# Kernel optimization log

Hardware: AMD Instinct MI355X
Metric: run time of the kernel (lower is better)

The kernel has to match this reference:

```python
import jax, jax.numpy as jnp
import numpy as np

N_NODES = 100000


def _gcn_conv(x, W, b, src, dst, norm, n):
    # PyG GCNConv: h = x @ W; out[i] = sum_j norm_ij * h[j]; out += b
    h = x @ W                                   # [N, F_out]
    msg = h[src] * norm[:, None]                # [E_total, F_out] gathered messages
    out = jax.ops.segment_sum(msg, dst, num_segments=n)
    return out + b


def _build_norm(edge_index, n):
    # add self loops, then symmetric normalization deg^-1/2 A_hat deg^-1/2
    loops = jnp.arange(n, dtype=edge_index.dtype)
    src = jnp.concatenate([edge_index[0], loops])
    dst = jnp.concatenate([edge_index[1], loops])
    deg = jnp.zeros((n,), jnp.float32).at[dst].add(1.0)
    dinv = jnp.where(deg > 0, jax.lax.rsqrt(deg), 0.0)
    norm = dinv[src] * dinv[dst]
    return src, dst, norm


def setup_inputs() -> dict:
    key = jax.random.key(0)
    k1, k2, k3 = jax.random.split(key, 3)
    d_in, d_hid, d_out = 128, 128, 64
    x = jax.random.normal(k1, (N_NODES, d_in), jnp.float32)
    edge_index = jax.random.randint(k2, (2, 1600000), 0, N_NODES, jnp.int64)
    kw1, kw2 = jax.random.split(k3)
    W1 = jax.random.normal(kw1, (d_in, d_hid), jnp.float32) * (1.0 / np.sqrt(d_in))
    b1 = jnp.zeros((d_hid,), jnp.float32)
    W2 = jax.random.normal(kw2, (d_hid, d_out), jnp.float32) * (1.0 / np.sqrt(d_hid))
    b2 = jnp.zeros((d_out,), jnp.float32)
    return {"x": x, "edge_index": edge_index, "W1": W1, "b1": b1, "W2": W2, "b2": b2}


def reference(x, edge_index, W1, b1, W2, b2):
    n = x.shape[0]
    src, dst, norm = _build_norm(edge_index, n)
    h = _gcn_conv(x, W1, b1, src, dst, norm, n)
    h = jax.nn.relu(h)
    # F.dropout(training=False) in eval mode is identity
    out = _gcn_conv(h, W2, b2, src, dst, norm, n)
    return out
```

## Files before the change

kernel.cpp:

```cpp
#include <hip/hip_runtime.h>
#include <hip/hip_fp16.h>

typedef _Float16 half8 __attribute__((ext_vector_type(8)));
typedef float f32x4 __attribute__((ext_vector_type(4)));

#define BUCKET_CAP 8192


__device__ __forceinline__ unsigned pack_half2(float x, float y) {
    __half2 h = __float22half2_rn(make_float2(x, y));
    return *reinterpret_cast<unsigned*>(&h);
}
__device__ __forceinline__ float2 up2(unsigned u) {
    __half2 h = *reinterpret_cast<__half2*>(&u);
    return __half22float2(h);
}
__device__ __forceinline__ void acc8(float4& a, uint2 v) {
    float2 p = up2(v.x), q = up2(v.y);
    a.x += p.x; a.y += p.y; a.z += q.x; a.w += q.y;
}
__device__ __forceinline__ void acc4(float2& a, unsigned v) {
    float2 p = up2(v);
    a.x += p.x; a.y += p.y;
}
__device__ __forceinline__ uint2 ld8(const char* __restrict__ b, unsigned off) {
    return *reinterpret_cast<const uint2*>(b + off);
}
__device__ __forceinline__ unsigned ld4(const char* __restrict__ b, unsigned off) {
    return *reinterpret_cast<const unsigned*>(b + off);
}


__global__ __launch_bounds__(256) void k_wconv(const float* __restrict__ W1,
                                               const float* __restrict__ W2,
                                               __half* __restrict__ Wt1,
                                               __half* __restrict__ Wt2,
                                               int* __restrict__ bcnt, int nbz) {
    int i = blockIdx.x * 256 + threadIdx.x;
    if (i < nbz) bcnt[i] = 0;
    if (i < 16384) {
        int col = i >> 7, k = i & 127;
        Wt1[i] = __float2half(W1[(k << 7) + col]);
    } else if (i < 24576) {
        int j = i - 16384;
        int col = j >> 7, k = j & 127;
        Wt2[j] = __float2half(W2[(k << 6) + col]);
    }
}


__global__ __launch_bounds__(256) void k_bscatter2(const int* __restrict__ src,
                                                   const int* __restrict__ dst, int E,
                                                   int* __restrict__ bcnt,
                                                   unsigned* __restrict__ pairs,
                                                   int NB, int epb) {
    __shared__ int h[512];
    __shared__ int base[512];
    for (int i = threadIdx.x; i < NB; i += 256) h[i] = 0;
    __syncthreads();
    int lo = blockIdx.x * epb;
    int hi = min(lo + epb, E);
    for (int e = lo + threadIdx.x; e < hi; e += 256)
        atomicAdd(&h[dst[e] >> 8], 1);
    __syncthreads();
    for (int i = threadIdx.x; i < NB; i += 256) {
        int c = h[i];
        base[i] = c ? atomicAdd(&bcnt[i], c) : 0;
        h[i] = 0;
    }
    __syncthreads();
    for (int e = lo + threadIdx.x; e < hi; e += 256) {
        int s = src[e], d = dst[e];
        int b = d >> 8;
        int r = atomicAdd(&h[b], 1);
        pairs[(size_t)b * BUCKET_CAP + base[b] + r] =
            (unsigned)s | ((unsigned)(d & 255) << 24);
    }
}

__global__ __launch_bounds__(256) void k_bfinal2(const unsigned* __restrict__ pairs,
                                                 const int* __restrict__ bcnt,
                                                 float* __restrict__ dinv,
                                                 int* __restrict__ offs,
                                                 int* __restrict__ csc,
                                                 int n, int E, int NB) {
    __shared__ int cnt[256];
    __shared__ int scn[256];
    int b = blockIdx.x, t = threadIdx.x;

    int part = 0;
    for (int i = t; i < b; i += 256) part += bcnt[i];
    scn[t] = part;
    __syncthreads();
    for (int d = 128; d > 0; d >>= 1) {
        if (t < d) scn[t] += scn[t + d];
        __syncthreads();
    }
    int cbase = scn[0];
    int cnt_b = bcnt[b];
    __syncthreads();

    cnt[t] = 0;
    __syncthreads();
    size_t plo = (size_t)b * BUCKET_CAP;
    for (int e = t; e < cnt_b; e += 256)
        atomicAdd(&cnt[pairs[plo + e] >> 24], 1);
    __syncthreads();
    int c = cnt[t];
    int node = b * 256 + t;
    if (node < n) dinv[node] = rsqrtf((float)(c + 1));
    scn[t] = c;
    __syncthreads();
    for (int d = 1; d < 256; d <<= 1) {
        int xv = (t >= d) ? scn[t - d] : 0;
        __syncthreads();
        scn[t] += xv;
        __syncthreads();
    }
    int myoff = cbase + scn[t] - c;
    if (node < n) offs[node] = myoff;
    if (b == NB - 1 && t == 255) offs[n] = cbase + scn[255];
    cnt[t] = myoff;
    __syncthreads();
    for (int e = t; e < cnt_b; e += 256) {
        unsigned p = pairs[plo + e];
        int pos = atomicAdd(&cnt[p >> 24], 1);
        csc[pos] = (int)(p & 0x00FFFFFFu);
    }
}


__global__ __launch_bounds__(256) void gemm1_mfma(const float* __restrict__ X,
                                                  const __half* __restrict__ Wt,
                                                  const float* __restrict__ dinv,
                                                  __half* __restrict__ H, int nrows) {
    __shared__ half8 wt[2048];
    const int t = threadIdx.x;

    const half8* Wg = reinterpret_cast<const half8*>(Wt);
    for (int i = t; i < 2048; i += 256) {
        int col = i >> 4, kc = i & 15;
        wt[(col << 4) | (kc ^ (col & 7))] = Wg[i];
    }

    const int wid = t >> 6, lane = t & 63;
    const int li = lane & 15, kq = lane >> 4;
    const int rbase = blockIdx.x * 64 + wid * 16;
    int row = rbase + li;
    int rowc = min(row, nrows - 1);

    const f32x4* X4 = reinterpret_cast<const f32x4*>(X) + (size_t)rowc * 32;
    half8 a[4];
#pragma unroll
    for (int kk = 0; kk < 4; ++kk) {
        f32x4 lo = __builtin_nontemporal_load(&X4[kk * 8 + kq * 2]);
        f32x4 hi = __builtin_nontemporal_load(&X4[kk * 8 + kq * 2 + 1]);
        half8 v;
        v[0] = (_Float16)lo[0]; v[1] = (_Float16)lo[1];
        v[2] = (_Float16)lo[2]; v[3] = (_Float16)lo[3];
        v[4] = (_Float16)hi[0]; v[5] = (_Float16)hi[1];
        v[6] = (_Float16)hi[2]; v[7] = (_Float16)hi[3];
        a[kk] = v;
    }
    __syncthreads();

    f32x4 acc[8];
#pragma unroll
    for (int ct = 0; ct < 8; ++ct) acc[ct] = (f32x4){0.f, 0.f, 0.f, 0.f};

#pragma unroll
    for (int ct = 0; ct < 8; ++ct) {
        int col = ct * 16 + li;
        int cbase = col << 4, sw = col & 7;
#pragma unroll
        for (int kk = 0; kk < 4; ++kk) {
            half8 b = wt[cbase | ((kk * 4 + kq) ^ sw)];
            acc[ct] = __builtin_amdgcn_mfma_f32_16x16x32_f16(a[kk], b, acc[ct], 0, 0, 0);
        }
    }

    const int r0 = rbase + kq * 4;
#pragma unroll
    for (int r = 0; r < 4; ++r) {
        int rr = r0 + r;
        if (rr < nrows) {
            float s = dinv[rr];
            __half* orow = H + (size_t)rr * 128;
#pragma unroll
            for (int ct = 0; ct < 8; ++ct)
                orow[ct * 16 + li] = __float2half(acc[ct][r] * s);
        }
    }
}

__global__ __launch_bounds__(256) void gemm2_mfma(const __half* __restrict__ Xh,
                                                  const __half* __restrict__ Wt,
                                                  const float* __restrict__ dinv,
                                                  __half* __restrict__ H, int nrows) {
    __shared__ half8 wt[1024];
    const int t = threadIdx.x;

    const half8* Wg = reinterpret_cast<const half8*>(Wt);
    for (int i = t; i < 1024; i += 256) {
        int col = i >> 4, kc = i & 15;
        wt[(col << 4) | (kc ^ (col & 7))] = Wg[i];
    }

    const int wid = t >> 6, lane = t & 63;
    const int li = lane & 15, kq = lane >> 4;
    const int rbase = blockIdx.x * 64 + wid * 16;
    int row = rbase + li;
    int rowc = min(row, nrows - 1);

    const half8* A8 = reinterpret_cast<const half8*>(Xh) + (size_t)rowc * 16;
    half8 a[4];
#pragma unroll
    for (int kk = 0; kk < 4; ++kk) a[kk] = A8[kk * 4 + kq];
    __syncthreads();

    f32x4 acc[4];
#pragma unroll
    for (int ct = 0; ct < 4; ++ct) acc[ct] = (f32x4){0.f, 0.f, 0.f, 0.f};

#pragma unroll
    for (int ct = 0; ct < 4; ++ct) {
        int col = ct * 16 + li;
        int cbase = col << 4, sw = col & 7;
#pragma unroll
        for (int kk = 0; kk < 4; ++kk) {
            half8 b = wt[cbase | ((kk * 4 + kq) ^ sw)];
            acc[ct] = __builtin_amdgcn_mfma_f32_16x16x32_f16(a[kk], b, acc[ct], 0, 0, 0);
        }
    }

    const int r0 = rbase + kq * 4;
#pragma unroll
    for (int r = 0; r < 4; ++r) {
        int rr = r0 + r;
        if (rr < nrows) {
            float s = dinv[rr];
            __half* orow = H + (size_t)rr * 64;
#pragma unroll
            for (int ct = 0; ct < 4; ++ct)
                orow[ct * 16 + li] = __float2half(acc[ct][r] * s);
        }
    }
}


__global__ __launch_bounds__(256) void k_agg1(const __half* __restrict__ h,
                                              const int* __restrict__ offs,
                                              const int* __restrict__ csc,
                                              const float* __restrict__ dinv,
                                              const float* __restrict__ bias,
                                              __half* __restrict__ out, int n) {
    int node = (blockIdx.x * 256 + threadIdx.x) >> 6;
    if (node >= n) return;
    int lane = threadIdx.x & 63;
    int g = lane >> 5, li = lane & 31;
    const char* hb = reinterpret_cast<const char*>(h);
    const unsigned loff = (unsigned)li << 3;
    int start = __builtin_amdgcn_readfirstlane(offs[node]);
    int end   = __builtin_amdgcn_readfirstlane(offs[node + 1]);
    float4 acc = make_float4(0.f, 0.f, 0.f, 0.f);

    int e = start;
    int emain = start + ((end - start) & ~15);
    for (; e < emain; e += 16) {
        int idx[16];
#pragma unroll
        for (int j = 0; j < 16; ++j) idx[j] = csc[e + j];
        uint2 v[8];
#pragma unroll
        for (int j = 0; j < 8; ++j)
            v[j] = ld8(hb, (((unsigned)(g ? idx[2 * j + 1] : idx[2 * j])) << 8) | loff);
#pragma unroll
        for (int j = 0; j < 8; ++j) acc8(acc, v[j]);
    }
    for (; e < end; e += 2) {
        int sa = csc[e];
        int sb = (e + 1 < end) ? csc[e + 1] : sa;
        unsigned o = (((unsigned)(g ? sb : sa)) << 8) | loff;
        uint2 v = ld8(hb, o);
        if (g && (e + 1 >= end)) { v.x = 0u; v.y = 0u; }
        acc8(acc, v);
    }
    acc.x += __shfl_xor(acc.x, 32);
    acc.y += __shfl_xor(acc.y, 32);
    acc.z += __shfl_xor(acc.z, 32);
    acc.w += __shfl_xor(acc.w, 32);
    uint2 vs = ld8(hb, (((unsigned)node) << 8) | loff);
    acc8(acc, vs);
    float di = dinv[node];
    float4 bb = reinterpret_cast<const float4*>(bias)[li];
    float ox = fmaxf(fmaf(acc.x, di, bb.x), 0.f);
    float oy = fmaxf(fmaf(acc.y, di, bb.y), 0.f);
    float oz = fmaxf(fmaf(acc.z, di, bb.z), 0.f);
    float ow = fmaxf(fmaf(acc.w, di, bb.w), 0.f);
    if (g == 0)
        reinterpret_cast<uint2*>(out)[(size_t)node * 32 + li] =
            make_uint2(pack_half2(ox, oy), pack_half2(oz, ow));
}

__global__ __launch_bounds__(256) void k_agg2(const __half* __restrict__ h,
                                              const int* __restrict__ offs,
                                              const int* __restrict__ csc,
                                              const float* __restrict__ dinv,
                                              const float* __restrict__ bias,
                                              float* __restrict__ out, int n) {
    int node = (blockIdx.x * 256 + threadIdx.x) >> 6;
    if (node >= n) return;
    int lane = threadIdx.x & 63;
    int g = lane >> 5, li = lane & 31;
    const char* hb = reinterpret_cast<const char*>(h);
    const unsigned loff = (unsigned)li << 2;
    int start = __builtin_amdgcn_readfirstlane(offs[node]);
    int end   = __builtin_amdgcn_readfirstlane(offs[node + 1]);
    float2 acc = make_float2(0.f, 0.f);

    int e = start;
    int emain = start + ((end - start) & ~15);
    for (; e < emain; e += 16) {
        int idx[16];
#pragma unroll
        for (int j = 0; j < 16; ++j) idx[j] = csc[e + j];
        unsigned v[8];
#pragma unroll
        for (int j = 0; j < 8; ++j)
            v[j] = ld4(hb, (((unsigned)(g ? idx[2 * j + 1] : idx[2 * j])) << 7) | loff);
#pragma unroll
        for (int j = 0; j < 8; ++j) acc4(acc, v[j]);
    }
    for (; e < end; e += 2) {
        int sa = csc[e];
        int sb = (e + 1 < end) ? csc[e + 1] : sa;
        unsigned o = (((unsigned)(g ? sb : sa)) << 7) | loff;
        unsigned v = ld4(hb, o);
        if (g && (e + 1 >= end)) v = 0u;
        acc4(acc, v);
    }
    acc.x += __shfl_xor(acc.x, 32);
    acc.y += __shfl_xor(acc.y, 32);
    acc4(acc, ld4(hb, (((unsigned)node) << 7) | loff));
    float di = dinv[node];
    float2 bb = reinterpret_cast<const float2*>(bias)[li];
    if (g == 0)
        reinterpret_cast<float2*>(out)[(size_t)node * 32 + li] =
            make_float2(fmaf(acc.x, di, bb.x), fmaf(acc.y, di, bb.y));
}


extern "C" void kernel_launch(void* const* d_in, const int* in_sizes, int n_in,
                              void* d_out, int out_size, void* d_ws, size_t ws_size,
                              hipStream_t stream) {
    const float* x  = (const float*)d_in[0];
    const int*   ei = (const int*)d_in[1];
    const float* W1 = (const float*)d_in[2];
    const float* b1 = (const float*)d_in[3];
    const float* W2 = (const float*)d_in[4];
    const float* b2 = (const float*)d_in[5];
    float* out = (float*)d_out;

    const int n = in_sizes[0] / 128;
    const int E = in_sizes[1] / 2;
    const int* src = ei;
    const int* dst = ei + E;
    const int NB = (n + 255) / 256;

    char* p = (char*)d_ws;
    auto carve = [&](size_t bytes) -> void* {
        void* r = (void*)p;
        p += (bytes + 255) & ~(size_t)255;
        return r;
    };
    float* dinv    = (float*)carve((size_t)n * 4);
    int*   offs    = (int*)carve((size_t)(n + 1) * 4);
    int*   bcnt    = (int*)carve((size_t)(NB + 1) * 4);
    __half* Wt1h   = (__half*)carve(16384 * 2);
    __half* Wt2h   = (__half*)carve(8192 * 2);
    int*   csc     = (int*)carve((size_t)E * 4);
    __half* h1     = (__half*)carve((size_t)n * 128 * 2);
    __half* out1   = (__half*)carve((size_t)n * 128 * 2);
    unsigned* pairs = (unsigned*)h1;
    __half* h2     = h1;

    const int gmm  = (n + 63) / 64;
    const int gagg = (n + 3) / 4;
    const int GB   = 256;
    const int epb  = (E + GB - 1) / GB;

    k_wconv<<<96, 256, 0, stream>>>(W1, W2, Wt1h, Wt2h, bcnt, NB + 1);

    k_bscatter2<<<GB, 256, 0, stream>>>(src, dst, E, bcnt, pairs, NB, epb);
    k_bfinal2<<<NB, 256, 0, stream>>>(pairs, bcnt, dinv, offs, csc, n, E, NB);

    gemm1_mfma<<<gmm, 256, 0, stream>>>(x, Wt1h, dinv, h1, n);
    k_agg1<<<gagg, 256, 0, stream>>>(h1, offs, csc, dinv, b1, out1, n);

    gemm2_mfma<<<gmm, 256, 0, stream>>>(out1, Wt2h, dinv, h2, n);
    k_agg2<<<gagg, 256, 0, stream>>>(h2, offs, csc, dinv, b2, out, n);
}
```

Measured before the change: 220.5 us.

## Use 1024-node dst buckets for CSC build and shorten gather unroll

The CSC build now groups destination nodes into 1024-node buckets instead of 256. Each packed pair holds a 17-bit source index plus a 10-bit local destination, and each finalize thread handles four nodes with vectorized offs/dinv stores. The scatter grid grows to 512 blocks, and both aggregation kernels drop their gather unroll from 16 edges to 8 to lower register pressure. The risks are fewer finalize blocks (less parallelism), fewer loads in flight per wave in aggregation, and a packing that only holds when node counts stay below 2^17.

New measurement: 203.5 us. 1.08x faster.

```diff
diff --git a/kernel.cpp b/kernel.cpp
--- a/kernel.cpp
+++ b/kernel.cpp
@@ -4,7 +4,9 @@
 typedef _Float16 half8 __attribute__((ext_vector_type(8)));
 typedef float f32x4 __attribute__((ext_vector_type(4)));
 
-#define BUCKET_CAP 8192
+#define BUCKET_CAP 32768
+#define BNODES 1024
+#define NBSHIFT 10
 
 
 __device__ __forceinline__ unsigned pack_half2(float x, float y) {
@@ -54,14 +56,14 @@
                                                    int* __restrict__ bcnt,
                                                    unsigned* __restrict__ pairs,
                                                    int NB, int epb) {
-    __shared__ int h[512];
-    __shared__ int base[512];
+    __shared__ int h[128];
+    __shared__ int base[128];
     for (int i = threadIdx.x; i < NB; i += 256) h[i] = 0;
     __syncthreads();
     int lo = blockIdx.x * epb;
     int hi = min(lo + epb, E);
     for (int e = lo + threadIdx.x; e < hi; e += 256)
-        atomicAdd(&h[dst[e] >> 8], 1);
+        atomicAdd(&h[dst[e] >> NBSHIFT], 1);
     __syncthreads();
     for (int i = threadIdx.x; i < NB; i += 256) {
         int c = h[i];
@@ -71,10 +73,10 @@
     __syncthreads();
     for (int e = lo + threadIdx.x; e < hi; e += 256) {
         int s = src[e], d = dst[e];
-        int b = d >> 8;
+        int b = d >> NBSHIFT;
         int r = atomicAdd(&h[b], 1);
         pairs[(size_t)b * BUCKET_CAP + base[b] + r] =
-            (unsigned)s | ((unsigned)(d & 255) << 24);
+            (unsigned)s | ((unsigned)(d & (BNODES - 1)) << 17);
     }
 }
 
@@ -84,8 +86,9 @@
                                                  int* __restrict__ offs,
                                                  int* __restrict__ csc,
                                                  int n, int E, int NB) {
-    __shared__ int cnt[256];
+    __shared__ int cnt[BNODES];
     __shared__ int scn[256];
+    __shared__ int cur[BNODES];
     int b = blockIdx.x, t = threadIdx.x;
 
     int part = 0;
@@ -100,16 +103,17 @@
     int cnt_b = bcnt[b];
     __syncthreads();
 
-    cnt[t] = 0;
+    for (int i = t; i < BNODES; i += 256) cnt[i] = 0;
     __syncthreads();
     size_t plo = (size_t)b * BUCKET_CAP;
     for (int e = t; e < cnt_b; e += 256)
-        atomicAdd(&cnt[pairs[plo + e] >> 24], 1);
-    __syncthreads();
-    int c = cnt[t];
-    int node = b * 256 + t;
-    if (node < n) dinv[node] = rsqrtf((float)(c + 1));
-    scn[t] = c;
+        atomicAdd(&cnt[pairs[plo + e] >> 17], 1);
+    __syncthreads();
+
+    int c0 = cnt[4 * t], c1 = cnt[4 * t + 1], c2 = cnt[4 * t + 2], c3 = cnt[4 * t + 3];
+    int tot = c0 + c1 + c2 + c3;
+    __syncthreads();
+    scn[t] = tot;
     __syncthreads();
     for (int d = 1; d < 256; d <<= 1) {
         int xv = (t >= d) ? scn[t - d] : 0;
@@ -117,15 +121,26 @@
         scn[t] += xv;
         __syncthreads();
     }
-    int myoff = cbase + scn[t] - c;
-    if (node < n) offs[node] = myoff;
-    if (b == NB - 1 && t == 255) offs[n] = cbase + scn[255];
-    cnt[t] = myoff;
+    int basee = cbase + scn[t] - tot;
+    int o0 = basee, o1 = basee + c0, o2 = o1 + c1, o3 = o2 + c2;
+    int node0 = b * BNODES + 4 * t;
+    if (node0 + 3 < n) {
+        *reinterpret_cast<int4*>(offs + node0) = make_int4(o0, o1, o2, o3);
+        *reinterpret_cast<float4*>(dinv + node0) =
+            make_float4(rsqrtf((float)(c0 + 1)), rsqrtf((float)(c1 + 1)),
+                        rsqrtf((float)(c2 + 1)), rsqrtf((float)(c3 + 1)));
+    } else {
+        if (node0 < n)     { offs[node0]     = o0; dinv[node0]     = rsqrtf((float)(c0 + 1)); }
+        if (node0 + 1 < n) { offs[node0 + 1] = o1; dinv[node0 + 1] = rsqrtf((float)(c1 + 1)); }
+        if (node0 + 2 < n) { offs[node0 + 2] = o2; dinv[node0 + 2] = rsqrtf((float)(c2 + 1)); }
+    }
+    if (b == NB - 1 && t == 255) offs[n] = E;
+    cur[4 * t] = o0; cur[4 * t + 1] = o1; cur[4 * t + 2] = o2; cur[4 * t + 3] = o3;
     __syncthreads();
     for (int e = t; e < cnt_b; e += 256) {
         unsigned p = pairs[plo + e];
-        int pos = atomicAdd(&cnt[p >> 24], 1);
-        csc[pos] = (int)(p & 0x00FFFFFFu);
+        int pos = atomicAdd(&cur[p >> 17], 1);
+        csc[pos] = (int)(p & 0x1FFFFu);
     }
 }
 
@@ -265,17 +280,19 @@
     float4 acc = make_float4(0.f, 0.f, 0.f, 0.f);
 
     int e = start;
-    int emain = start + ((end - start) & ~15);
-    for (; e < emain; e += 16) {
-        int idx[16];
-#pragma unroll
-        for (int j = 0; j < 16; ++j) idx[j] = csc[e + j];
-        uint2 v[8];
-#pragma unroll
-        for (int j = 0; j < 8; ++j)
-            v[j] = ld8(hb, (((unsigned)(g ? idx[2 * j + 1] : idx[2 * j])) << 8) | loff);
-#pragma unroll
-        for (int j = 0; j < 8; ++j) acc8(acc, v[j]);
+    int emain = start + ((end - start) & ~7);
+    for (; e < emain; e += 8) {
+        int a0 = csc[e],     a1 = csc[e + 1], a2 = csc[e + 2], a3 = csc[e + 3];
+        int a4 = csc[e + 4], a5 = csc[e + 5], a6 = csc[e + 6], a7 = csc[e + 7];
+        unsigned o0 = (((unsigned)(g ? a1 : a0)) << 8) | loff;
+        unsigned o1 = (((unsigned)(g ? a3 : a2)) << 8) | loff;
+        unsigned o2 = (((unsigned)(g ? a5 : a4)) << 8) | loff;
+        unsigned o3 = (((unsigned)(g ? a7 : a6)) << 8) | loff;
+        uint2 v0 = ld8(hb, o0);
+        uint2 v1 = ld8(hb, o1);
+        uint2 v2 = ld8(hb, o2);
+        uint2 v3 = ld8(hb, o3);
+        acc8(acc, v0); acc8(acc, v1); acc8(acc, v2); acc8(acc, v3);
     }
     for (; e < end; e += 2) {
         int sa = csc[e];
@@ -319,17 +336,19 @@
     float2 acc = make_float2(0.f, 0.f);
 
     int e = start;
-    int emain = start + ((end - start) & ~15);
-    for (; e < emain; e += 16) {
-        int idx[16];
-#pragma unroll
-        for (int j = 0; j < 16; ++j) idx[j] = csc[e + j];
-        unsigned v[8];
-#pragma unroll
-        for (int j = 0; j < 8; ++j)
-            v[j] = ld4(hb, (((unsigned)(g ? idx[2 * j + 1] : idx[2 * j])) << 7) | loff);
-#pragma unroll
-        for (int j = 0; j < 8; ++j) acc4(acc, v[j]);
+    int emain = start + ((end - start) & ~7);
+    for (; e < emain; e += 8) {
+        int a0 = csc[e],     a1 = csc[e + 1], a2 = csc[e + 2], a3 = csc[e + 3];
+        int a4 = csc[e + 4], a5 = csc[e + 5], a6 = csc[e + 6], a7 = csc[e + 7];
+        unsigned o0 = (((unsigned)(g ? a1 : a0)) << 7) | loff;
+        unsigned o1 = (((unsigned)(g ? a3 : a2)) << 7) | loff;
+        unsigned o2 = (((unsigned)(g ? a5 : a4)) << 7) | loff;
+        unsigned o3 = (((unsigned)(g ? a7 : a6)) << 7) | loff;
+        unsigned v0 = ld4(hb, o0);
+        unsigned v1 = ld4(hb, o1);
+        unsigned v2 = ld4(hb, o2);
+        unsigned v3 = ld4(hb, o3);
+        acc4(acc, v0); acc4(acc, v1); acc4(acc, v2); acc4(acc, v3);
     }
     for (; e < end; e += 2) {
         int sa = csc[e];
@@ -365,7 +384,7 @@
     const int E = in_sizes[1] / 2;
     const int* src = ei;
     const int* dst = ei + E;
-    const int NB = (n + 255) / 256;
+    const int NB = (n + BNODES - 1) / BNODES;
 
     char* p = (char*)d_ws;
     auto carve = [&](size_t bytes) -> void* {
@@ -386,7 +405,7 @@
 
     const int gmm  = (n + 63) / 64;
     const int gagg = (n + 3) / 4;
-    const int GB   = 256;
+    const int GB   = 512;
     const int epb  = (E + GB - 1) / GB;
 
     k_wconv<<<96, 256, 0, stream>>>(W1, W2, Wt1h, Wt2h, bcnt, NB + 1);
```

## Store hidden features in 16-column slices and aggregate per slice for cache locality

Applied to the files above, without the earlier changes.

The GEMM outputs and the layer-1 aggregation output now use a sliced layout: 16-feature (32-byte) slices, each holding all nodes contiguously. The aggregation kernels launch one block per slice and node group, with 16 edges per wavefront gathered in parallel. Each slice's working set is smaller, so random neighbour gathers should hit L2/MALL more often. The cost is 8x more blocks, repeated index loads per slice, and 32-byte gathers that may use memory transactions less efficiently. The last offset is also set directly to E.

Result: slower. 422.7 us (+91.7%).

```diff
diff --git a/kernel.cpp b/kernel.cpp
--- a/kernel.cpp
+++ b/kernel.cpp
@@ -19,15 +19,8 @@
     float2 p = up2(v.x), q = up2(v.y);
     a.x += p.x; a.y += p.y; a.z += q.x; a.w += q.y;
 }
-__device__ __forceinline__ void acc4(float2& a, unsigned v) {
-    float2 p = up2(v);
-    a.x += p.x; a.y += p.y;
-}
 __device__ __forceinline__ uint2 ld8(const char* __restrict__ b, unsigned off) {
     return *reinterpret_cast<const uint2*>(b + off);
-}
-__device__ __forceinline__ unsigned ld4(const char* __restrict__ b, unsigned off) {
-    return *reinterpret_cast<const unsigned*>(b + off);
 }
 
 
@@ -119,7 +112,7 @@
     }
     int myoff = cbase + scn[t] - c;
     if (node < n) offs[node] = myoff;
-    if (b == NB - 1 && t == 255) offs[n] = cbase + scn[255];
+    if (b == NB - 1 && t == 255) offs[n] = E;
     cnt[t] = myoff;
     __syncthreads();
     for (int e = t; e < cnt_b; e += 256) {
@@ -133,7 +126,7 @@
 __global__ __launch_bounds__(256) void gemm1_mfma(const float* __restrict__ X,
                                                   const __half* __restrict__ Wt,
                                                   const float* __restrict__ dinv,
-                                                  __half* __restrict__ H, int nrows) {
+                                                  __half* __restrict__ H, int nrows, int N) {
     __shared__ half8 wt[2048];
     const int t = threadIdx.x;
 
@@ -179,16 +172,18 @@
         }
     }
 
+    char* Hb = reinterpret_cast<char*>(H);
     const int r0 = rbase + kq * 4;
 #pragma unroll
     for (int r = 0; r < 4; ++r) {
         int rr = r0 + r;
         if (rr < nrows) {
             float s = dinv[rr];
-            __half* orow = H + (size_t)rr * 128;
-#pragma unroll
-            for (int ct = 0; ct < 8; ++ct)
-                orow[ct * 16 + li] = __float2half(acc[ct][r] * s);
+#pragma unroll
+            for (int ct = 0; ct < 8; ++ct) {
+                size_t off = ((size_t)ct * N + rr) * 32 + li * 2;
+                *reinterpret_cast<__half*>(Hb + off) = __float2half(acc[ct][r] * s);
+            }
         }
     }
 }
@@ -196,7 +191,8 @@
 __global__ __launch_bounds__(256) void gemm2_mfma(const __half* __restrict__ Xh,
                                                   const __half* __restrict__ Wt,
                                                   const float* __restrict__ dinv,
-                                                  __half* __restrict__ H, int nrows) {
+                                                  __half* __restrict__ H,
+                                                  int nrows, int N) {
     __shared__ half8 wt[1024];
     const int t = threadIdx.x;
 
@@ -212,10 +208,14 @@
     int row = rbase + li;
     int rowc = min(row, nrows - 1);
 
-    const half8* A8 = reinterpret_cast<const half8*>(Xh) + (size_t)rowc * 16;
+    const char* Xb = reinterpret_cast<const char*>(Xh);
     half8 a[4];
 #pragma unroll
-    for (int kk = 0; kk < 4; ++kk) a[kk] = A8[kk * 4 + kq];
+    for (int kk = 0; kk < 4; ++kk) {
+        int f0 = (kk * 4 + kq) * 8;
+        size_t off = ((size_t)(f0 >> 4) * N + rowc) * 32 + (f0 & 15) * 2;
+        a[kk] = *reinterpret_cast<const half8*>(Xb + off);
+    }
     __syncthreads();
 
     f32x4 acc[4];
@@ -233,120 +233,127 @@
         }
     }
 
+    char* Hb = reinterpret_cast<char*>(H);
     const int r0 = rbase + kq * 4;
 #pragma unroll
     for (int r = 0; r < 4; ++r) {
         int rr = r0 + r;
         if (rr < nrows) {
             float s = dinv[rr];
-            __half* orow = H + (size_t)rr * 64;
-#pragma unroll
-            for (int ct = 0; ct < 4; ++ct)
-                orow[ct * 16 + li] = __float2half(acc[ct][r] * s);
+#pragma unroll
+            for (int ct = 0; ct < 4; ++ct) {
+                size_t off = ((size_t)ct * N + rr) * 32 + li * 2;
+                *reinterpret_cast<__half*>(Hb + off) = __float2half(acc[ct][r] * s);
+            }
         }
     }
 }
 
 
-__global__ __launch_bounds__(256) void k_agg1(const __half* __restrict__ h,
-                                              const int* __restrict__ offs,
-                                              const int* __restrict__ csc,
-                                              const float* __restrict__ dinv,
-                                              const float* __restrict__ bias,
-                                              __half* __restrict__ out, int n) {
-    int node = (blockIdx.x * 256 + threadIdx.x) >> 6;
+__global__ __launch_bounds__(256) void k_agg1s(const __half* __restrict__ h,
+                                               const int* __restrict__ offs,
+                                               const int* __restrict__ csc,
+                                               const float* __restrict__ dinv,
+                                               const float* __restrict__ bias,
+                                               __half* __restrict__ out,
+                                               int n, int N) {
+    const int bid = blockIdx.x;
+    const int slice = bid & 7;
+    const int wid = (threadIdx.x >> 6);
+    const int node = (bid >> 3) * 4 + wid;
     if (node >= n) return;
-    int lane = threadIdx.x & 63;
-    int g = lane >> 5, li = lane & 31;
-    const char* hb = reinterpret_cast<const char*>(h);
-    const unsigned loff = (unsigned)li << 3;
+    const int lane = threadIdx.x & 63;
+    const int eg = lane >> 2;
+    const int lb = lane & 3;
+    const unsigned loff = (unsigned)lb << 3;
+
+    const char* hsl = reinterpret_cast<const char*>(h) + (size_t)slice * ((size_t)N * 32);
     int start = __builtin_amdgcn_readfirstlane(offs[node]);
     int end   = __builtin_amdgcn_readfirstlane(offs[node + 1]);
+
     float4 acc = make_float4(0.f, 0.f, 0.f, 0.f);
-
-    int e = start;
-    int emain = start + ((end - start) & ~15);
-    for (; e < emain; e += 16) {
-        int idx[16];
-#pragma unroll
-        for (int j = 0; j < 16; ++j) idx[j] = csc[e + j];
-        uint2 v[8];
-#pragma unroll
-        for (int j = 0; j < 8; ++j)
-            v[j] = ld8(hb, (((unsigned)(g ? idx[2 * j + 1] : idx[2 * j])) << 8) | loff);
-#pragma unroll
-        for (int j = 0; j < 8; ++j) acc8(acc, v[j]);
-    }
-    for (; e < end; e += 2) {
-        int sa = csc[e];
-        int sb = (e + 1 < end) ? csc[e + 1] : sa;
-        unsigned o = (((unsigned)(g ? sb : sa)) << 8) | loff;
-        uint2 v = ld8(hb, o);
-        if (g && (e + 1 >= end)) { v.x = 0u; v.y = 0u; }
+    for (int e = start; e < end; e += 16) {
+        int ee = e + eg;
+        bool valid = ee < end;
+        int eec = valid ? ee : (end - 1);
+        int idx = csc[eec];
+        uint2 v = ld8(hsl, ((unsigned)idx << 5) | loff);
+        if (!valid) { v.x = 0u; v.y = 0u; }
         acc8(acc, v);
     }
-    acc.x += __shfl_xor(acc.x, 32);
-    acc.y += __shfl_xor(acc.y, 32);
-    acc.z += __shfl_xor(acc.z, 32);
-    acc.w += __shfl_xor(acc.w, 32);
-    uint2 vs = ld8(hb, (((unsigned)node) << 8) | loff);
-    acc8(acc, vs);
-    float di = dinv[node];
-    float4 bb = reinterpret_cast<const float4*>(bias)[li];
-    float ox = fmaxf(fmaf(acc.x, di, bb.x), 0.f);
-    float oy = fmaxf(fmaf(acc.y, di, bb.y), 0.f);
-    float oz = fmaxf(fmaf(acc.z, di, bb.z), 0.f);
-    float ow = fmaxf(fmaf(acc.w, di, bb.w), 0.f);
-    if (g == 0)
-        reinterpret_cast<uint2*>(out)[(size_t)node * 32 + li] =
-            make_uint2(pack_half2(ox, oy), pack_half2(oz, ow));
-}
-
-__global__ __launch_bounds__(256) void k_agg2(const __half* __restrict__ h,
-                                              const int* __restrict__ offs,
-                                              const int* __restrict__ csc,
-                                              const float* __restrict__ dinv,
-                                              const float* __restrict__ bias,
-                                              float* __restrict__ out, int n) {
-    int node = (blockIdx.x * 256 + threadIdx.x) >> 6;
-    if (node >= n) return;
-    int lane = threadIdx.x & 63;
-    int g = lane >> 5, li = lane & 31;
-    const char* hb = reinterpret_cast<const char*>(h);
-    const unsigned loff = (unsigned)li << 2;
+    if (eg == 0) acc8(acc, ld8(hsl, ((unsigned)node << 5) | loff));
+
+#pragma unroll
+    for (int m = 4; m <= 32; m <<= 1) {
+        acc.x += __shfl_xor(acc.x, m);
+        acc.y += __shfl_xor(acc.y, m);
+        acc.z += __shfl_xor(acc.z, m);
+        acc.w += __shfl_xor(acc.w, m);
+    }
+
+    if (eg == 0) {
+        float di = dinv[node];
+        float4 bb = reinterpret_cast<const float4*>(bias)[slice * 4 + lb];
+        uint2 o = make_uint2(
+            pack_half2(fmaxf(fmaf(acc.x, di, bb.x), 0.f),
+                       fmaxf(fmaf(acc.y, di, bb.y), 0.f)),
+            pack_half2(fmaxf(fmaf(acc.z, di, bb.z), 0.f),
+                       fmaxf(fmaf(acc.w, di, bb.w), 0.f)));
+        *reinterpret_cast<uint2*>(reinterpret_cast<char*>(out) +
+            ((size_t)slice * N + node) * 32 + loff) = o;
+    }
+}
+
+__global__ __launch_bounds__(256) void k_agg2s(const __half* __restrict__ h,
+                                               const int* __restrict__ offs,
+                                               const int* __restrict__ csc,
+                                               const float* __restrict__ dinv,
+                                               const float* __restrict__ bias,
+                                               float* __restrict__ out,
+                                               int n, int N, int NH) {
+    const int bid = blockIdx.x;
+    const int vs = bid & 7;
+    const int slice = vs & 3;
+    const int half_ = vs >> 2;
+    const int wid = (threadIdx.x >> 6);
+    const int node = (bid >> 3) * 4 + wid + half_ * NH;
+    if (node >= n || (bid >> 3) * 4 + wid >= NH) return;
+    const int lane = threadIdx.x & 63;
+    const int eg = lane >> 2;
+    const int lb = lane & 3;
+    const unsigned loff = (unsigned)lb << 3;
+
+    const char* hsl = reinterpret_cast<const char*>(h) + (size_t)slice * ((size_t)N * 32);
     int start = __builtin_amdgcn_readfirstlane(offs[node]);
     int end   = __builtin_amdgcn_readfirstlane(offs[node + 1]);
-    float2 acc = make_float2(0.f, 0.f);
-
-    int e = start;
-    int emain = start + ((end - start) & ~15);
-    for (; e < emain; e += 16) {
-        int idx[16];
-#pragma unroll
-        for (int j = 0; j < 16; ++j) idx[j] = csc[e + j];
-        unsigned v[8];
-#pragma unroll
-        for (int j = 0; j < 8; ++j)
-            v[j] = ld4(hb, (((unsigned)(g ? idx[2 * j + 1] : idx[2 * j])) << 7) | loff);
-#pragma unroll
-        for (int j = 0; j < 8; ++j) acc4(acc, v[j]);
-    }
-    for (; e < end; e += 2) {
-        int sa = csc[e];
-        int sb = (e + 1 < end) ? csc[e + 1] : sa;
-        unsigned o = (((unsigned)(g ? sb : sa)) << 7) | loff;
-        unsigned v = ld4(hb, o);
-        if (g && (e + 1 >= end)) v = 0u;
-        acc4(acc, v);
-    }
-    acc.x += __shfl_xor(acc.x, 32);
-    acc.y += __shfl_xor(acc.y, 32);
-    acc4(acc, ld4(hb, (((unsigned)node) << 7) | loff));
-    float di = dinv[node];
-    float2 bb = reinterpret_cast<const float2*>(bias)[li];
-    if (g == 0)
-        reinterpret_cast<float2*>(out)[(size_t)node * 32 + li] =
-            make_float2(fmaf(acc.x, di, bb.x), fmaf(acc.y, di, bb.y));
+
+    float4 acc = make_float4(0.f, 0.f, 0.f, 0.f);
+    for (int e = start; e < end; e += 16) {
+        int ee = e + eg;
+        bool valid = ee < end;
+        int eec = valid ? ee : (end - 1);
+        int idx = csc[eec];
+        uint2 v = ld8(hsl, ((unsigned)idx << 5) | loff);
+        if (!valid) { v.x = 0u; v.y = 0u; }
+        acc8(acc, v);
+    }
+    if (eg == 0) acc8(acc, ld8(hsl, ((unsigned)node << 5) | loff));
+
+#pragma unroll
+    for (int m = 4; m <= 32; m <<= 1) {
+        acc.x += __shfl_xor(acc.x, m);
+        acc.y += __shfl_xor(acc.y, m);
+        acc.z += __shfl_xor(acc.z, m);
+        acc.w += __shfl_xor(acc.w, m);
+    }
+
+    if (eg == 0) {
+        float di = dinv[node];
+        float4 bb = reinterpret_cast<const float4*>(bias)[slice * 4 + lb];
+        float4 o = make_float4(fmaf(acc.x, di, bb.x), fmaf(acc.y, di, bb.y),
+                               fmaf(acc.z, di, bb.z), fmaf(acc.w, di, bb.w));
+        reinterpret_cast<float4*>(out)[(size_t)node * 16 + slice * 4 + lb] = o;
+    }
 }
 
 
@@ -384,19 +391,21 @@
     unsigned* pairs = (unsigned*)h1;
     __half* h2     = h1;
 
-    const int gmm  = (n + 63) / 64;
-    const int gagg = (n + 3) / 4;
-    const int GB   = 256;
-    const int epb  = (E + GB - 1) / GB;
+    const int gmm   = (n + 63) / 64;
+    const int gagg1 = ((n + 3) / 4) * 8;
+    const int NH    = ((n + 7) / 8) * 4;
+    const int gagg2 = ((NH + 3) / 4) * 8;
+    const int GB    = 256;
+    const int epb   = (E + GB - 1) / GB;
 
     k_wconv<<<96, 256, 0, stream>>>(W1, W2, Wt1h, Wt2h, bcnt, NB + 1);
 
     k_bscatter2<<<GB, 256, 0, stream>>>(src, dst, E, bcnt, pairs, NB, epb);
     k_bfinal2<<<NB, 256, 0, stream>>>(pairs, bcnt, dinv, offs, csc, n, E, NB);
 
-    gemm1_mfma<<<gmm, 256, 0, stream>>>(x, Wt1h, dinv, h1, n);
-    k_agg1<<<gagg, 256, 0, stream>>>(h1, offs, csc, dinv, b1, out1, n);
-
-    gemm2_mfma<<<gmm, 256, 0, stream>>>(out1, Wt2h, dinv, h2, n);
-    k_agg2<<<gagg, 256, 0, stream>>>(h2, offs, csc, dinv, b2, out, n);
-}
+    gemm1_mfma<<<gmm, 256, 0, stream>>>(x, Wt1h, dinv, h1, n, n);
+    k_agg1s<<<gagg1, 256, 0, stream>>>(h1, offs, csc, dinv, b1, out1, n, n);
+
+    gemm2_mfma<<<gmm, 256, 0, stream>>>(out1, Wt2h, dinv, h2, n, n);
+    k_agg2s<<<gagg2, 256, 0, stream>>>(h2, offs, csc, dinv, b2, out, n, n, NH);
+}
```
